# Optimization experiments

Hardware: AMD Instinct MI355X
Metric: run time of the kernel (lower is better)

## Reference

```python
import jax, jax.numpy as jnp
import numpy as np

RADIUS = 8
EPS = 1e-4


def window_sum(x, rh, rw):
    # sliding-window sum with edge-truncated windows, via cumsum+slice+concat
    ch = jnp.cumsum(x, axis=2)
    wh = 2 * rh + 1
    top = ch[..., rh:wh, :]
    midh = ch[..., wh:, :] - ch[..., :-wh, :]
    bot = ch[..., -1:, :] - ch[..., -wh:-rh - 1, :]
    out = jnp.concatenate([top, midh, bot], axis=2)
    cw = jnp.cumsum(out, axis=3)
    ww = 2 * rw + 1
    left = cw[..., rw:ww]
    midw = cw[..., ww:] - cw[..., :-ww]
    right = cw[..., -1:] - cw[..., -ww:-rw - 1]
    return jnp.concatenate([left, midw, right], axis=3)


def box_mean(x, r):
    # normalized box filter: window sum / per-pixel valid count
    return window_sum(x, r, r) / window_sum(jnp.ones_like(x), r, r)


def setup_inputs() -> dict:
    key = jax.random.key(0)
    k1, k2, k3 = jax.random.split(key, 3)
    p_lr = jax.random.uniform(k1, (8, 3, 256, 256), dtype=jnp.float32)
    I_lr = jax.random.uniform(k2, (8, 3, 256, 256), dtype=jnp.float32)
    I_hr = jax.random.uniform(k3, (8, 3, 1024, 1024), dtype=jnp.float32)
    return {"p_lr": p_lr, "I_lr": I_lr, "I_hr": I_hr}


def reference(p_lr, I_lr, I_hr):
    r = RADIUS
    mean_I = box_mean(I_lr, r)
    mean_p = box_mean(p_lr, r)
    cov_Ip = box_mean(I_lr * p_lr, r) - mean_I * mean_p
    var_I = box_mean(I_lr * I_lr, r) - mean_I ** 2
    A_lr = cov_Ip / (var_I + EPS)
    B_lr = mean_p - A_lr * mean_I
    N, C = I_hr.shape[0], I_hr.shape[1]
    H, W = I_hr.shape[2], I_hr.shape[3]
    # bilinear, half-pixel centers == torch align_corners=False
    A_hr = jax.image.resize(A_lr, (N, C, H, W), method="linear")
    B_hr = jax.image.resize(B_lr, (N, C, H, W), method="linear")
    return A_hr * I_hr + B_hr
```

## Files before the change

kernel.cpp:

```cpp
#include <hip/hip_runtime.h>

#define RADIUS 8
#define LR 256
#define HRES 1024
#define NC 24
#define GF_EPS 1e-4f
#define STRIP 4

typedef float f4 __attribute__((ext_vector_type(4)));

__global__ __launch_bounds__(256) void kH(const float* __restrict__ p,
                                          const float* __restrict__ I,
                                          float* __restrict__ hI, float* __restrict__ hp,
                                          float* __restrict__ hIp, float* __restrict__ hII) {
    __shared__ float sI[LR];
    __shared__ float sp[LR];
    const int g = blockIdx.x;
    const int x = threadIdx.x;
    const int base = g * LR;
    sI[x] = I[base + x];
    sp[x] = p[base + x];
    __syncthreads();
    float aI = 0.f, ap = 0.f, aIp = 0.f, aII = 0.f;
    const int lo = max(x - RADIUS, 0);
    const int hi = min(x + RADIUS, LR - 1);
    #pragma unroll 1
    for (int xx = lo; xx <= hi; ++xx) {
        const float vi = sI[xx];
        const float vp = sp[xx];
        aI  += vi;
        ap  += vp;
        aIp += vi * vp;
        aII += vi * vi;
    }
    hI[base + x]  = aI;
    hp[base + x]  = ap;
    hIp[base + x] = aIp;
    hII[base + x] = aII;
}

__global__ __launch_bounds__(256) void kV(const float* __restrict__ hI, const float* __restrict__ hp,
                                          const float* __restrict__ hIp, const float* __restrict__ hII,
                                          float* __restrict__ A, float* __restrict__ B) {
    const int x     = threadIdx.x;
    const int img   = blockIdx.x / (LR / STRIP);
    const int strip = blockIdx.x % (LR / STRIP);
    const int y0    = strip * STRIP;
    const int ib    = img * LR * LR;

    float sI = 0.f, sp_ = 0.f, sIp = 0.f, sII = 0.f;
    #pragma unroll 1
    for (int yy = y0 - RADIUS; yy <= y0 + RADIUS; ++yy) {
        if (yy >= 0 && yy < LR) {
            const int idx = ib + yy * LR + x;
            sI  += hI[idx];
            sp_ += hp[idx];
            sIp += hIp[idx];
            sII += hII[idx];
        }
    }
    const int cntx = min(x + RADIUS, LR - 1) - max(x - RADIUS, 0) + 1;
    #pragma unroll
    for (int y = y0; y < y0 + STRIP; ++y) {
        const int cnty = min(y + RADIUS, LR - 1) - max(y - RADIUS, 0) + 1;
        const float inv = 1.0f / (float)(cntx * cnty);
        const float mI  = sI  * inv;
        const float mp  = sp_ * inv;
        const float mIp = sIp * inv;
        const float mII = sII * inv;
        const float cov = mIp - mI * mp;
        const float var = mII - mI * mI;
        const float a   = cov / (var + GF_EPS);
        const float b   = mp - a * mI;
        const int idx = ib + y * LR + x;
        A[idx] = a;
        B[idx] = b;
        const int yadd = y + RADIUS + 1;
        const int ysub = y - RADIUS;
        if (yadd < LR) {
            const int ia = ib + yadd * LR + x;
            sI += hI[ia]; sp_ += hp[ia]; sIp += hIp[ia]; sII += hII[ia];
        }
        if (ysub >= 0) {
            const int is = ib + ysub * LR + x;
            sI -= hI[is]; sp_ -= hp[is]; sIp -= hIp[is]; sII -= hII[is];
        }
    }
}

__global__ __launch_bounds__(256) void kR(const float* __restrict__ A, const float* __restrict__ B,
                                          const float* __restrict__ Ihr, float* __restrict__ out) {
    __shared__ float av[8][LR];
    __shared__ float bv[8][LR];

    const int blk = blockIdx.x;
    const int img = blk >> 7;
    const int k2  = blk & 127;
    const int k   = k2 << 1;
    const int tx  = threadIdx.x;

    const float* Ai = A + img * LR * LR;
    const float* Bi = B + img * LR * LR;
    const int rm = max(k - 1, 0);
    const int rp = min(k + 2, LR - 1);

    const float aU = Ai[rm * LR + tx];
    const float a0 = Ai[k * LR + tx];
    const float a1 = Ai[(k + 1) * LR + tx];
    const float aD = Ai[rp * LR + tx];
    const float bU = Bi[rm * LR + tx];
    const float b0 = Bi[k * LR + tx];
    const float b1 = Bi[(k + 1) * LR + tx];
    const float bD = Bi[rp * LR + tx];

    av[0][tx] = aU + 0.625f * (a0 - aU);
    av[1][tx] = aU + 0.875f * (a0 - aU);
    av[2][tx] = a0 + 0.125f * (a1 - a0);
    av[3][tx] = a0 + 0.375f * (a1 - a0);
    av[4][tx] = a0 + 0.625f * (a1 - a0);
    av[5][tx] = a0 + 0.875f * (a1 - a0);
    av[6][tx] = a1 + 0.125f * (aD - a1);
    av[7][tx] = a1 + 0.375f * (aD - a1);
    bv[0][tx] = bU + 0.625f * (b0 - bU);
    bv[1][tx] = bU + 0.875f * (b0 - bU);
    bv[2][tx] = b0 + 0.125f * (b1 - b0);
    bv[3][tx] = b0 + 0.375f * (b1 - b0);
    bv[4][tx] = b0 + 0.625f * (b1 - b0);
    bv[5][tx] = b0 + 0.875f * (b1 - b0);
    bv[6][tx] = b1 + 0.125f * (bD - b1);
    bv[7][tx] = b1 + 0.375f * (bD - b1);
    __syncthreads();

    const long long base = ((long long)img << 20) + ((long long)k << 12) + (tx << 2);

    f4 ih[8];
    #pragma unroll
    for (int r = 0; r < 8; ++r)
        ih[r] = __builtin_nontemporal_load((const f4*)(Ihr + base + ((long long)r << 10)));

    const int cm1 = max(tx - 1, 0);
    const int cp1 = min(tx + 1, LR - 1);

    #pragma unroll
    for (int r = 0; r < 8; ++r) {
        const float am = av[r][cm1], ac = av[r][tx], ap = av[r][cp1];
        const float bm = bv[r][cm1], bc = bv[r][tx], bp = bv[r][cp1];
        float p0, p1, q0, q1;
        if (tx == 0) { p0 = ac; p1 = ac; q0 = bc; q1 = bc; }
        else {
            p0 = am + 0.625f * (ac - am);
            p1 = am + 0.875f * (ac - am);
            q0 = bm + 0.625f * (bc - bm);
            q1 = bm + 0.875f * (bc - bm);
        }
        const float p2 = ac + 0.125f * (ap - ac);
        const float p3 = ac + 0.375f * (ap - ac);
        const float q2 = bc + 0.125f * (bp - bc);
        const float q3 = bc + 0.375f * (bp - bc);

        f4 res;
        res.x = p0 * ih[r].x + q0;
        res.y = p1 * ih[r].y + q1;
        res.z = p2 * ih[r].z + q2;
        res.w = p3 * ih[r].w + q3;
        __builtin_nontemporal_store(res, (f4*)(out + base + ((long long)r << 10)));
    }
}

extern "C" void kernel_launch(void* const* d_in, const int* in_sizes, int n_in,
                              void* d_out, int out_size, void* d_ws, size_t ws_size,
                              hipStream_t stream) {
    const float* p_lr = (const float*)d_in[0];
    const float* I_lr = (const float*)d_in[1];
    const float* I_hr = (const float*)d_in[2];
    float* out = (float*)d_out;
    float* ws  = (float*)d_ws;

    const int S = NC * LR * LR;
    float* hI  = ws + 0 * (size_t)S;
    float* hp  = ws + 1 * (size_t)S;
    float* hIp = ws + 2 * (size_t)S;
    float* hII = ws + 3 * (size_t)S;
    float* A   = ws + 4 * (size_t)S;
    float* B   = ws + 5 * (size_t)S;

    kH<<<NC * LR, 256, 0, stream>>>(p_lr, I_lr, hI, hp, hIp, hII);
    kV<<<NC * (LR / STRIP), 256, 0, stream>>>(hI, hp, hIp, hII, A, B);
    kR<<<NC * 128, 256, 0, stream>>>(A, B, I_hr, out);
}
```

Baseline: 212.1 us.

## Fuse horizontal and vertical box-filter passes into one kernel

Merges the horizontal and vertical box-sum kernels into a single kernel. It keeps vertical running sums of I, p, I*p and I*I in registers and does the horizontal window sum from a double-buffered shared-memory row. This removes four full-size intermediate arrays and one launch, cutting global memory traffic in the low-res stage. The cost is a barrier per row, 17-tap shared-memory reads per quantity, and fewer blocks (strip of 8 rows).

```diff
diff --git a/kernel.cpp b/kernel.cpp
--- a/kernel.cpp
+++ b/kernel.cpp
@@ -5,86 +5,80 @@
 #define HRES 1024
 #define NC 24
 #define GF_EPS 1e-4f
-#define STRIP 4
+#define FSTRIP 8
 
 typedef float f4 __attribute__((ext_vector_type(4)));
 
-__global__ __launch_bounds__(256) void kH(const float* __restrict__ p,
+__global__ __launch_bounds__(256) void kF(const float* __restrict__ p,
                                           const float* __restrict__ I,
-                                          float* __restrict__ hI, float* __restrict__ hp,
-                                          float* __restrict__ hIp, float* __restrict__ hII) {
-    __shared__ float sI[LR];
-    __shared__ float sp[LR];
-    const int g = blockIdx.x;
-    const int x = threadIdx.x;
-    const int base = g * LR;
-    sI[x] = I[base + x];
-    sp[x] = p[base + x];
-    __syncthreads();
-    float aI = 0.f, ap = 0.f, aIp = 0.f, aII = 0.f;
-    const int lo = max(x - RADIUS, 0);
-    const int hi = min(x + RADIUS, LR - 1);
-    #pragma unroll 1
-    for (int xx = lo; xx <= hi; ++xx) {
-        const float vi = sI[xx];
-        const float vp = sp[xx];
-        aI  += vi;
-        ap  += vp;
-        aIp += vi * vp;
-        aII += vi * vi;
-    }
-    hI[base + x]  = aI;
-    hp[base + x]  = ap;
-    hIp[base + x] = aIp;
-    hII[base + x] = aII;
-}
-
-__global__ __launch_bounds__(256) void kV(const float* __restrict__ hI, const float* __restrict__ hp,
-                                          const float* __restrict__ hIp, const float* __restrict__ hII,
                                           float* __restrict__ A, float* __restrict__ B) {
+    __shared__ float vI[2][LR], vp[2][LR], vIp[2][LR], vII[2][LR];
     const int x     = threadIdx.x;
-    const int img   = blockIdx.x / (LR / STRIP);
-    const int strip = blockIdx.x % (LR / STRIP);
-    const int y0    = strip * STRIP;
+    const int img   = blockIdx.x >> 5;
+    const int strip = blockIdx.x & 31;
+    const int y0    = strip * FSTRIP;
     const int ib    = img * LR * LR;
+    const float* Ii = I + ib;
+    const float* pi = p + ib;
 
     float sI = 0.f, sp_ = 0.f, sIp = 0.f, sII = 0.f;
     #pragma unroll 1
     for (int yy = y0 - RADIUS; yy <= y0 + RADIUS; ++yy) {
         if (yy >= 0 && yy < LR) {
-            const int idx = ib + yy * LR + x;
-            sI  += hI[idx];
-            sp_ += hp[idx];
-            sIp += hIp[idx];
-            sII += hII[idx];
+            const float vi = Ii[yy * LR + x];
+            const float vq = pi[yy * LR + x];
+            sI  += vi;
+            sp_ += vq;
+            sIp += vi * vq;
+            sII += vi * vi;
         }
     }
     const int cntx = min(x + RADIUS, LR - 1) - max(x - RADIUS, 0) + 1;
-    #pragma unroll
-    for (int y = y0; y < y0 + STRIP; ++y) {
-        const int cnty = min(y + RADIUS, LR - 1) - max(y - RADIUS, 0) + 1;
-        const float inv = 1.0f / (float)(cntx * cnty);
-        const float mI  = sI  * inv;
-        const float mp  = sp_ * inv;
-        const float mIp = sIp * inv;
-        const float mII = sII * inv;
-        const float cov = mIp - mI * mp;
-        const float var = mII - mI * mI;
-        const float a   = cov / (var + GF_EPS);
-        const float b   = mp - a * mI;
-        const int idx = ib + y * LR + x;
-        A[idx] = a;
-        B[idx] = b;
+
+    #pragma unroll 2
+    for (int k = 0; k < FSTRIP; ++k) {
+        const int y   = y0 + k;
+        const int buf = k & 1;
+        vI [buf][x] = sI;
+        vp [buf][x] = sp_;
+        vIp[buf][x] = sIp;
+        vII[buf][x] = sII;
+        __syncthreads();
+
         const int yadd = y + RADIUS + 1;
         const int ysub = y - RADIUS;
-        if (yadd < LR) {
-            const int ia = ib + yadd * LR + x;
-            sI += hI[ia]; sp_ += hp[ia]; sIp += hIp[ia]; sII += hII[ia];
+        float aI = 0.f, aq = 0.f, rI = 0.f, rq = 0.f;
+        if (yadd < LR) { aI = Ii[yadd * LR + x]; aq = pi[yadd * LR + x]; }
+        if (ysub >= 0) { rI = Ii[ysub * LR + x]; rq = pi[ysub * LR + x]; }
+
+        float hI = 0.f, hp = 0.f, hIp = 0.f, hII = 0.f;
+        #pragma unroll
+        for (int t = -RADIUS; t <= RADIUS; ++t) {
+            const int   xt = x + t;
+            const int   xx = min(max(xt, 0), LR - 1);
+            const float m  = ((unsigned)xt < (unsigned)LR) ? 1.f : 0.f;
+            hI  = fmaf(m, vI [buf][xx], hI);
+            hp  = fmaf(m, vp [buf][xx], hp);
+            hIp = fmaf(m, vIp[buf][xx], hIp);
+            hII = fmaf(m, vII[buf][xx], hII);
         }
-        if (ysub >= 0) {
-            const int is = ib + ysub * LR + x;
-            sI -= hI[is]; sp_ -= hp[is]; sIp -= hIp[is]; sII -= hII[is];
-        }
+
+        const int   cnty = min(y + RADIUS, LR - 1) - max(y - RADIUS, 0) + 1;
+        const float inv  = 1.0f / (float)(cntx * cnty);
+        const float mI   = hI * inv;
+        const float mp   = hp * inv;
+        const float cov  = hIp * inv - mI * mp;
+        const float var  = hII * inv - mI * mI;
+        const float a    = cov / (var + GF_EPS);
+        const float bb   = mp - a * mI;
+        const int   idx  = ib + y * LR + x;
+        A[idx] = a;
+        B[idx] = bb;
+
+        sI  += aI - rI;
+        sp_ += aq - rq;
+        sIp += fmaf(aI, aq, -rI * rq);
+        sII += fmaf(aI, aI, -rI * rI);
     }
 }
 
@@ -177,14 +171,9 @@
     float* ws  = (float*)d_ws;
 
     const int S = NC * LR * LR;
-    float* hI  = ws + 0 * (size_t)S;
-    float* hp  = ws + 1 * (size_t)S;
-    float* hIp = ws + 2 * (size_t)S;
-    float* hII = ws + 3 * (size_t)S;
-    float* A   = ws + 4 * (size_t)S;
-    float* B   = ws + 5 * (size_t)S;
+    float* A = ws + 0 * (size_t)S;
+    float* B = ws + 1 * (size_t)S;
 
-    kH<<<NC * LR, 256, 0, stream>>>(p_lr, I_lr, hI, hp, hIp, hII);
-    kV<<<NC * (LR / STRIP), 256, 0, stream>>>(hI, hp, hIp, hII, A, B);
+    kF<<<NC * (LR / FSTRIP), 256, 0, stream>>>(p_lr, I_lr, A, B);
     kR<<<NC * 128, 256, 0, stream>>>(A, B, I_hr, out);
 }
```

New measurement: 200.3 us. 1.06x faster.
